# Kernel tuning notes

Hardware: AMD Instinct MI355X
Metric: run time of the kernel (lower is better)

The kernel has to match this reference:

```python
import jax, jax.numpy as jnp
import numpy as np

N, E, IN_C, HID, OUT_C, HEADS, NUM_CLASSES = 50000, 800000, 128, 64, 64, 4, 40
NEG_SLOPE = 0.2


def _gat_conv(x, src, dst, W, a_src, a_dst, bias, heads, concat):
    # x: [N, F_in]; W: [F_in, heads*C]; a_src/a_dst: [1, heads, C]; bias: [out]
    n = x.shape[0]
    h = (x @ W).reshape(n, heads, -1)                      # [N, H, C]
    alpha_s = (h * a_src).sum(-1)                          # [N, H]
    alpha_d = (h * a_dst).sum(-1)                          # [N, H]
    e = jax.nn.leaky_relu(alpha_s[src] + alpha_d[dst], NEG_SLOPE)  # [E, H]
    # scatter-softmax over incoming edges of each dst node
    emax = jax.ops.segment_max(e, dst, num_segments=n)
    emax = jnp.where(jnp.isfinite(emax), emax, 0.0)
    ee = jnp.exp(e - emax[dst])
    denom = jax.ops.segment_sum(ee, dst, num_segments=n) + 1e-16
    w = ee / denom[dst]                                    # [E, H]
    out = jax.ops.segment_sum(h[src] * w[:, :, None], dst, num_segments=n)  # [N, H, C]
    out = out.reshape(n, -1) if concat else out.mean(axis=1)
    return out + bias


def setup_inputs() -> dict:
    key = jax.random.key(0)
    ks = jax.random.split(key, 12)
    s1 = 1.0 / np.sqrt(IN_C)
    s2 = 1.0 / np.sqrt(HID * HEADS)
    s3 = 1.0 / np.sqrt(OUT_C)
    return {
        "x": jax.random.normal(ks[0], (N, IN_C), dtype=jnp.float32),
        "edge_index": jax.random.randint(ks[1], (2, E), 0, N, dtype=jnp.int64),
        "W1": jax.random.normal(ks[2], (IN_C, HEADS * HID), dtype=jnp.float32) * s1,
        "att_src1": jax.random.normal(ks[3], (1, HEADS, HID), dtype=jnp.float32) * s1,
        "att_dst1": jax.random.normal(ks[4], (1, HEADS, HID), dtype=jnp.float32) * s1,
        "b1": jnp.zeros((HEADS * HID,), dtype=jnp.float32),
        "W2": jax.random.normal(ks[5], (HEADS * HID, OUT_C), dtype=jnp.float32) * s2,
        "att_src2": jax.random.normal(ks[6], (1, 1, OUT_C), dtype=jnp.float32) * s2,
        "att_dst2": jax.random.normal(ks[7], (1, 1, OUT_C), dtype=jnp.float32) * s2,
        "b2": jnp.zeros((OUT_C,), dtype=jnp.float32),
        "fc_w": jax.random.normal(ks[8], (OUT_C, NUM_CLASSES), dtype=jnp.float32) * s3,
        "fc_b": jnp.zeros((NUM_CLASSES,), dtype=jnp.float32),
    }


def reference(x, edge_index, W1, att_src1, att_dst1, b1, W2, att_src2, att_dst2, b2, fc_w, fc_b):
    n = x.shape[0]
    loops = jnp.arange(n, dtype=edge_index.dtype)
    ei = jnp.concatenate([edge_index, jnp.stack([loops, loops])], axis=1)  # add self-loops (PyG default)
    src, dst = ei[0], ei[1]
    h = jax.nn.relu(_gat_conv(x, src, dst, W1, att_src1, att_dst1, b1, HEADS, True))
    h = jax.nn.relu(_gat_conv(h, src, dst, W2, att_src2, att_dst2, b2, 1, False))
    # dropout p=0.01 is identity in eval mode
    pooled = h.mean(axis=0, keepdims=True)                 # global mean pool -> [1, OUT_C]
    logits = pooled @ fc_w + fc_b
    return jax.nn.log_softmax(logits, axis=1)
```

## Files before the change

kernel.cpp:

```cpp
#include <hip/hip_runtime.h>
#include <hip/hip_bf16.h>
#include <math.h>

#define NEG_SLOPE 0.2f
#define CHUNK2 2048
#define PGROUPS 32

typedef __attribute__((ext_vector_type(8))) short bf16x8;
typedef __attribute__((ext_vector_type(4))) float f32x4;
typedef __attribute__((ext_vector_type(2))) float f32x2_t;

__device__ __forceinline__ float lrelu(float a) { return a >= 0.f ? a : NEG_SLOPE * a; }
__device__ __forceinline__ unsigned short f2bu(float v) {
  unsigned u = __float_as_uint(v);
  u += 0x7fffu + ((u >> 16) & 1u);
  return (unsigned short)(u >> 16);
}
__device__ __forceinline__ unsigned char f2fp8(float v) {
  return (unsigned char)(__builtin_amdgcn_cvt_pk_fp8_f32(v, v, 0, false) & 0xFF);
}
__device__ __forceinline__ void fp8x4_dec(unsigned v, float& a, float& b, float& c, float& d) {
  f32x2_t lo = __builtin_amdgcn_cvt_pk_f32_fp8(v, false);
  f32x2_t hi = __builtin_amdgcn_cvt_pk_f32_fp8(v, true);
  a = lo.x; b = lo.y; c = hi.x; d = hi.y;
}

__global__ __launch_bounds__(256) void prep_kernel(
    const float4* __restrict__ x4, ushort4* __restrict__ xb4, int nx4,
    const float* __restrict__ W1, unsigned short* __restrict__ w1t,
    const float* __restrict__ W2, unsigned short* __restrict__ w2t,
    const int* __restrict__ ei, int* __restrict__ bhist, int E0, int Etot, int NBUCK,
    int castBlocks, int wBlocks, int histBlocks) {
  __shared__ int hsm[256];
  int t = threadIdx.x;
  if (blockIdx.x < (unsigned)castBlocks) {
    for (int i = blockIdx.x * 256 + t; i < nx4; i += castBlocks * 256) {
      float4 v = x4[i];
      xb4[i] = make_ushort4(f2bu(v.x), f2bu(v.y), f2bu(v.z), f2bu(v.w));
    }
  } else if (blockIdx.x < (unsigned)(castBlocks + wBlocks)) {
    int bid = blockIdx.x - castBlocks;
    const int tot1 = 128 * 256, tot2 = 256 * 64;
    for (int i = bid * 256 + t; i < tot1 + tot2; i += wBlocks * 256) {
      if (i < tot1) { int k = i >> 8, n = i & 255; w1t[n * 128 + k] = f2bu(W1[i]); }
      else { int j = i - tot1; int k = j >> 6, n = j & 63; w2t[n * 256 + k] = f2bu(W2[j]); }
    }
  } else {
    int bid = blockIdx.x - castBlocks - wBlocks;
    hsm[t] = 0;
    __syncthreads();
    for (int e = bid * 256 + t; e < Etot; e += histBlocks * 256) {
      int dst = (e < E0) ? ei[E0 + e] : (e - E0);
      atomicAdd(&hsm[dst >> 8], 1);
    }
    __syncthreads();
    if (t < NBUCK && hsm[t]) atomicAdd(&bhist[t], hsm[t]);
  }
}

__global__ __launch_bounds__(256) void bucket_scan_kernel(const int* __restrict__ bhist,
    int* __restrict__ bucketOff, int* __restrict__ cursor, int* __restrict__ rowptrN,
    int NBUCK, int Etot) {
  __shared__ int s[256];
  int t = threadIdx.x;
  int v = (t < NBUCK) ? bhist[t] : 0;
  s[t] = v;
  __syncthreads();
  for (int off = 1; off < 256; off <<= 1) {
    int u = (t >= off) ? s[t - off] : 0;
    __syncthreads();
    s[t] += u;
    __syncthreads();
  }
  int excl = s[t] - v;
  if (t < NBUCK) { bucketOff[t] = excl; cursor[t] = excl; }
  if (t == 0) { bucketOff[NBUCK] = Etot; *rowptrN = Etot; }
}

__device__ void gemm_tile(const unsigned short* __restrict__ A,
    const unsigned short* __restrict__ BT, unsigned char* __restrict__ C8,
    const float* __restrict__ att_s, const float* __restrict__ att_d,
    float* __restrict__ as_, float* __restrict__ ad_,
    int M, int K, int Ncol, int H, int bx, int by, char* smem) {
  unsigned short (*Al)[40] = (unsigned short (*)[40])smem;
  unsigned short (*Bt)[40] = (unsigned short (*)[40])(smem + 5120);
  float* sal = (float*)(smem + 10240);
  float* sad = (float*)(smem + 10752);
  const int tid = threadIdx.x;
  const int row0 = by * 64, col0 = bx * 64;
  const int lane = tid & 63, wave = tid >> 6;
  const int wm = wave >> 1, wn = wave & 1;
  const int l15 = lane & 15, q = lane >> 4;

  f32x4 acc[2][2] = {};

  const int rr = tid >> 2, rc = (tid & 3) * 8;

  for (int k0 = 0; k0 < K; k0 += 32) {
    ushort4 av0 = make_ushort4(0, 0, 0, 0), av1 = av0;
    if (row0 + rr < M) {
      const ushort4* ap = (const ushort4*)(A + (size_t)(row0 + rr) * K + k0 + rc);
      av0 = ap[0]; av1 = ap[1];
    }
    *(ushort4*)&Al[rr][rc] = av0;
    *(ushort4*)&Al[rr][rc + 4] = av1;
    {
      const ushort4* bp = (const ushort4*)(BT + (size_t)(col0 + rr) * K + k0 + rc);
      *(ushort4*)&Bt[rr][rc] = bp[0];
      *(ushort4*)&Bt[rr][rc + 4] = bp[1];
    }
    __syncthreads();
    bf16x8 af[2], bf[2];
#pragma unroll
    for (int mi = 0; mi < 2; mi++)
      af[mi] = *(const bf16x8*)&Al[wm * 32 + mi * 16 + l15][q * 8];
#pragma unroll
    for (int ni = 0; ni < 2; ni++)
      bf[ni] = *(const bf16x8*)&Bt[wn * 32 + ni * 16 + l15][q * 8];
#pragma unroll
    for (int mi = 0; mi < 2; mi++)
#pragma unroll
      for (int ni = 0; ni < 2; ni++)
        acc[mi][ni] = __builtin_amdgcn_mfma_f32_16x16x32_bf16(af[mi], bf[ni], acc[mi][ni], 0, 0, 0);
    __syncthreads();
  }
#pragma unroll
  for (int mi = 0; mi < 2; mi++) {
#pragma unroll
    for (int r = 0; r < 4; r++) {
      int grow = row0 + wm * 32 + mi * 16 + q * 4 + r;
      if (grow < M) {
#pragma unroll
        for (int ni = 0; ni < 2; ni++) {
          int gcol = col0 + wn * 32 + ni * 16 + l15;
          C8[(size_t)grow * Ncol + gcol] = f2fp8(acc[mi][ni][r]);
        }
      }
    }
  }
  float atts0 = att_s[col0 + wn * 32 + l15];
  float atts1 = att_s[col0 + wn * 32 + 16 + l15];
  float attd0 = att_d[col0 + wn * 32 + l15];
  float attd1 = att_d[col0 + wn * 32 + 16 + l15];
#pragma unroll
  for (int mi = 0; mi < 2; mi++) {
#pragma unroll
    for (int r = 0; r < 4; r++) {
      float vs = acc[mi][0][r] * atts0 + acc[mi][1][r] * atts1;
      float vd = acc[mi][0][r] * attd0 + acc[mi][1][r] * attd1;
#pragma unroll
      for (int off = 1; off < 16; off <<= 1) {
        vs += __shfl_xor(vs, off);
        vd += __shfl_xor(vd, off);
      }
      if (l15 == 0) {
        int rl = wm * 32 + mi * 16 + q * 4 + r;
        sal[wn * 64 + rl] = vs;
        sad[wn * 64 + rl] = vd;
      }
    }
  }
  __syncthreads();
  if (tid < 64) {
    int grow = row0 + tid;
    if (grow < M) {
      as_[(size_t)grow * H + bx] = sal[tid] + sal[64 + tid];
      ad_[(size_t)grow * H + bx] = sad[tid] + sad[64 + tid];
    }
  }
}

__global__ __launch_bounds__(256) void gemm_alpha_kernel(const unsigned short* __restrict__ A,
    const unsigned short* __restrict__ BT, unsigned char* __restrict__ C8,
    const float* __restrict__ att_s, const float* __restrict__ att_d,
    float* __restrict__ as_, float* __restrict__ ad_, int M, int K, int Ncol, int H) {
  __shared__ __align__(16) char smem[11264];
  gemm_tile(A, BT, C8, att_s, att_d, as_, ad_, M, K, Ncol, H, blockIdx.x, blockIdx.y, smem);
}

__global__ __launch_bounds__(256) void gemm1_scatter_kernel(
    const unsigned short* __restrict__ A, const unsigned short* __restrict__ BT,
    unsigned char* __restrict__ C8, const float* __restrict__ att_s,
    const float* __restrict__ att_d, float* __restrict__ as_, float* __restrict__ ad_,
    int M, int K, int Ncol, int H, int GX,
    const int* __restrict__ ei, int* __restrict__ cursor, int* __restrict__ pairs,
    int E0, int Etot, int NBUCK, int NSC) {
  __shared__ __align__(16) char smem[18432];
  if (blockIdx.x < (unsigned)NSC) {
    int2* stage = (int2*)smem;
    int* h = (int*)(smem + 16384);
    int* base = (int*)(smem + 17408);
    int t = threadIdx.x;
    int e0 = blockIdx.x * CHUNK2;
    h[t] = 0;
    __syncthreads();
    int cnt = Etot - e0;
    if (cnt > CHUNK2) cnt = CHUNK2;
    for (int i = t; i < cnt; i += 256) {
      int e = e0 + i;
      int s, d;
      if (e < E0) { s = ei[e]; d = ei[E0 + e]; } else { s = d = e - E0; }
      stage[i] = make_int2((s << 8) | (d & 255), d >> 8);
      atomicAdd(&h[d >> 8], 1);
    }
    __syncthreads();
    if (t < NBUCK && h[t]) base[t] = atomicAdd(&cursor[t], h[t]);
    __syncthreads();
    for (int i = t; i < cnt; i += 256) {
      int2 p = stage[i];
      int pos = atomicAdd(&base[p.y], 1);
      pairs[pos] = p.x;
    }
  } else {
    int flat = blockIdx.x - NSC;
    gemm_tile(A, BT, C8, att_s, att_d, as_, ad_, M, K, Ncol, H, flat % GX, flat / GX, smem);
  }
}

__global__ __launch_bounds__(256) void csr_build_kernel(const int* __restrict__ pairs,
    const int* __restrict__ bucketOff, int* __restrict__ rowptr, int* __restrict__ csr_src,
    int N) {
  int b = blockIdx.x, t = threadIdx.x;
  int base = bucketOff[b], cnt = bucketOff[b + 1] - base;
  int n0 = b << 8;
  __shared__ int h[256];
  __shared__ int s[256];
  __shared__ int ex[256];
  h[t] = 0;
  __syncthreads();
  for (int i = t; i < cnt; i += 256) atomicAdd(&h[pairs[base + i] & 255], 1);
  __syncthreads();
  int v = h[t];
  s[t] = v;
  __syncthreads();
  for (int off = 1; off < 256; off <<= 1) {
    int u = (t >= off) ? s[t - off] : 0;
    __syncthreads();
    s[t] += u;
    __syncthreads();
  }
  ex[t] = s[t] - v;
  if (n0 + t < N) rowptr[n0 + t] = base + ex[t];
  __syncthreads();
  for (int i = t; i < cnt; i += 256) {
    int p = pairs[base + i];
    int pos = atomicAdd(&ex[p & 255], 1);
    csr_src[base + pos] = ((unsigned)p) >> 8;
  }
}

__global__ __launch_bounds__(256) void aggr1_kernel(const int* __restrict__ rowptr,
    const int* __restrict__ csr_src, const float* __restrict__ as_,
    const float* __restrict__ ad_, const uint4* __restrict__ h1f8,
    const float* __restrict__ b1, unsigned short* __restrict__ out1, int Nn) {
  int lane = threadIdx.x & 63, wv = threadIdx.x >> 6;
  int q = lane >> 4, l15 = lane & 15;
  int n = (blockIdx.x * 4 + wv) * 4 + q;
  if (n >= Nn) return;
  int row = rowptr[n], deg = rowptr[n + 1] - row;
  int hh = l15 >> 2;
  float adv = ad_[n * 4 + hh];
  const uint4* hb = h1f8 + l15;
  float acc[16] = {};
  float wsum = 0.f;
  int s = 0;
  for (; s + 2 <= deg; s += 2) {
    int i0 = csr_src[row + s], i1 = csr_src[row + s + 1];
    float a0v = as_[i0 * 4 + hh], a1v = as_[i1 * 4 + hh];
    uint4 x0 = hb[(size_t)i0 * 16];
    uint4 x1 = hb[(size_t)i1 * 16];
    float w0 = __expf(lrelu(a0v + adv));
    float w1 = __expf(lrelu(a1v + adv));
    wsum += w0 + w1;
    float c0, c1, c2, c3;
    fp8x4_dec(x0.x, c0, c1, c2, c3);
    acc[0] = fmaf(w0, c0, acc[0]); acc[1] = fmaf(w0, c1, acc[1]);
    acc[2] = fmaf(w0, c2, acc[2]); acc[3] = fmaf(w0, c3, acc[3]);
    fp8x4_dec(x0.y, c0, c1, c2, c3);
    acc[4] = fmaf(w0, c0, acc[4]); acc[5] = fmaf(w0, c1, acc[5]);
    acc[6] = fmaf(w0, c2, acc[6]); acc[7] = fmaf(w0, c3, acc[7]);
    fp8x4_dec(x0.z, c0, c1, c2, c3);
    acc[8] = fmaf(w0, c0, acc[8]); acc[9] = fmaf(w0, c1, acc[9]);
    acc[10] = fmaf(w0, c2, acc[10]); acc[11] = fmaf(w0, c3, acc[11]);
    fp8x4_dec(x0.w, c0, c1, c2, c3);
    acc[12] = fmaf(w0, c0, acc[12]); acc[13] = fmaf(w0, c1, acc[13]);
    acc[14] = fmaf(w0, c2, acc[14]); acc[15] = fmaf(w0, c3, acc[15]);
    fp8x4_dec(x1.x, c0, c1, c2, c3);
    acc[0] = fmaf(w1, c0, acc[0]); acc[1] = fmaf(w1, c1, acc[1]);
    acc[2] = fmaf(w1, c2, acc[2]); acc[3] = fmaf(w1, c3, acc[3]);
    fp8x4_dec(x1.y, c0, c1, c2, c3);
    acc[4] = fmaf(w1, c0, acc[4]); acc[5] = fmaf(w1, c1, acc[5]);
    acc[6] = fmaf(w1, c2, acc[6]); acc[7] = fmaf(w1, c3, acc[7]);
    fp8x4_dec(x1.z, c0, c1, c2, c3);
    acc[8] = fmaf(w1, c0, acc[8]); acc[9] = fmaf(w1, c1, acc[9]);
    acc[10] = fmaf(w1, c2, acc[10]); acc[11] = fmaf(w1, c3, acc[11]);
    fp8x4_dec(x1.w, c0, c1, c2, c3);
    acc[12] = fmaf(w1, c0, acc[12]); acc[13] = fmaf(w1, c1, acc[13]);
    acc[14] = fmaf(w1, c2, acc[14]); acc[15] = fmaf(w1, c3, acc[15]);
  }
  if (s < deg) {
    int i0 = csr_src[row + s];
    float w0 = __expf(lrelu(as_[i0 * 4 + hh] + adv));
    wsum += w0;
    uint4 x0 = hb[(size_t)i0 * 16];
    float c0, c1, c2, c3;
    fp8x4_dec(x0.x, c0, c1, c2, c3);
    acc[0] = fmaf(w0, c0, acc[0]); acc[1] = fmaf(w0, c1, acc[1]);
    acc[2] = fmaf(w0, c2, acc[2]); acc[3] = fmaf(w0, c3, acc[3]);
    fp8x4_dec(x0.y, c0, c1, c2, c3);
    acc[4] = fmaf(w0, c0, acc[4]); acc[5] = fmaf(w0, c1, acc[5]);
    acc[6] = fmaf(w0, c2, acc[6]); acc[7] = fmaf(w0, c3, acc[7]);
    fp8x4_dec(x0.z, c0, c1, c2, c3);
    acc[8] = fmaf(w0, c0, acc[8]); acc[9] = fmaf(w0, c1, acc[9]);
    acc[10] = fmaf(w0, c2, acc[10]); acc[11] = fmaf(w0, c3, acc[11]);
    fp8x4_dec(x0.w, c0, c1, c2, c3);
    acc[12] = fmaf(w0, c0, acc[12]); acc[13] = fmaf(w0, c1, acc[13]);
    acc[14] = fmaf(w0, c2, acc[14]); acc[15] = fmaf(w0, c3, acc[15]);
  }
  float vinv = 1.f / wsum;
  int c0i = l15 * 16;
  unsigned short ob[16];
#pragma unroll
  for (int k = 0; k < 4; k++) {
    float4 bb = *(const float4*)(b1 + c0i + k * 4);
    float r0 = fmaf(acc[k * 4 + 0], vinv, bb.x);
    float r1 = fmaf(acc[k * 4 + 1], vinv, bb.y);
    float r2 = fmaf(acc[k * 4 + 2], vinv, bb.z);
    float r3 = fmaf(acc[k * 4 + 3], vinv, bb.w);
    ob[k * 4 + 0] = f2bu(r0 > 0.f ? r0 : 0.f);
    ob[k * 4 + 1] = f2bu(r1 > 0.f ? r1 : 0.f);
    ob[k * 4 + 2] = f2bu(r2 > 0.f ? r2 : 0.f);
    ob[k * 4 + 3] = f2bu(r3 > 0.f ? r3 : 0.f);
  }
  *(ushort4*)(out1 + (size_t)n * 256 + c0i) = *(ushort4*)&ob[0];
  *(ushort4*)(out1 + (size_t)n * 256 + c0i + 4) = *(ushort4*)&ob[4];
  *(ushort4*)(out1 + (size_t)n * 256 + c0i + 8) = *(ushort4*)&ob[8];
  *(ushort4*)(out1 + (size_t)n * 256 + c0i + 12) = *(ushort4*)&ob[12];
}

__global__ __launch_bounds__(256) void aggr2_pool_kernel(const int* __restrict__ rowptr,
    const int* __restrict__ csr_src, const float* __restrict__ as_,
    const float* __restrict__ ad_, const unsigned* __restrict__ h2f8,
    const float* __restrict__ b2, float* __restrict__ pooled_grp, int Nn) {
  int lane = threadIdx.x & 63, wv = threadIdx.x >> 6;
  int q = lane >> 4, l15 = lane & 15;
  int c0 = l15 * 4;
  const unsigned* hb = h2f8 + l15;
  float p0 = 0.f, p1 = 0.f, p2 = 0.f, p3 = 0.f;
  int stream = (blockIdx.x * 4 + wv) * 4 + q;
  int nstreams = gridDim.x * 16;
  for (int n = stream; n < Nn; n += nstreams) {
    int row = rowptr[n], deg = rowptr[n + 1] - row;
    float adv = ad_[n];
    float a0 = 0.f, a1 = 0.f, a2 = 0.f, a3 = 0.f, wsum = 0.f;
    int s = 0;
    for (; s + 8 <= deg; s += 8) {
      int idx[8];
      float al[8];
      unsigned xv[8];
#pragma unroll
      for (int j = 0; j < 8; j++) idx[j] = csr_src[row + s + j];
#pragma unroll
      for (int j = 0; j < 8; j++) al[j] = as_[idx[j]];
#pragma unroll
      for (int j = 0; j < 8; j++) xv[j] = hb[(size_t)idx[j] * 16];
#pragma unroll
      for (int j = 0; j < 8; j++) {
        float w = __expf(lrelu(al[j] + adv));
        wsum += w;
        float c0f, c1f, c2f, c3f;
        fp8x4_dec(xv[j], c0f, c1f, c2f, c3f);
        a0 = fmaf(w, c0f, a0); a1 = fmaf(w, c1f, a1);
        a2 = fmaf(w, c2f, a2); a3 = fmaf(w, c3f, a3);
      }
    }
    if (s + 4 <= deg) {
      int idx[4];
      float al[4];
      unsigned xv[4];
#pragma unroll
      for (int j = 0; j < 4; j++) idx[j] = csr_src[row + s + j];
#pragma unroll
      for (int j = 0; j < 4; j++) al[j] = as_[idx[j]];
#pragma unroll
      for (int j = 0; j < 4; j++) xv[j] = hb[(size_t)idx[j] * 16];
#pragma unroll
      for (int j = 0; j < 4; j++) {
        float w = __expf(lrelu(al[j] + adv));
        wsum += w;
        float c0f, c1f, c2f, c3f;
        fp8x4_dec(xv[j], c0f, c1f, c2f, c3f);
        a0 = fmaf(w, c0f, a0); a1 = fmaf(w, c1f, a1);
        a2 = fmaf(w, c2f, a2); a3 = fmaf(w, c3f, a3);
      }
      s += 4;
    }
    for (; s < deg; s++) {
      int i0 = csr_src[row + s];
      float w = __expf(lrelu(as_[i0] + adv));
      wsum += w;
      float c0f, c1f, c2f, c3f;
      fp8x4_dec(hb[(size_t)i0 * 16], c0f, c1f, c2f, c3f);
      a0 = fmaf(w, c0f, a0); a1 = fmaf(w, c1f, a1);
      a2 = fmaf(w, c2f, a2); a3 = fmaf(w, c3f, a3);
    }
    float vinv = 1.f / wsum;
    float4 bb = *(const float4*)(b2 + c0);
    float r0 = fmaf(a0, vinv, bb.x), r1 = fmaf(a1, vinv, bb.y);
    float r2 = fmaf(a2, vinv, bb.z), r3 = fmaf(a3, vinv, bb.w);
    p0 += r0 > 0.f ? r0 : 0.f; p1 += r1 > 0.f ? r1 : 0.f;
    p2 += r2 > 0.f ? r2 : 0.f; p3 += r3 > 0.f ? r3 : 0.f;
  }
  __shared__ float4 sred[4][4][16];
  sred[wv][q][l15] = make_float4(p0, p1, p2, p3);
  __syncthreads();
  if (threadIdx.x < 64) {
    int slot = threadIdx.x >> 2, comp = threadIdx.x & 3;
    float acc = 0.f;
#pragma unroll
    for (int i = 0; i < 4; i++)
#pragma unroll
      for (int j = 0; j < 4; j++) {
        float4 v = sred[i][j][slot];
        acc += comp == 0 ? v.x : (comp == 1 ? v.y : (comp == 2 ? v.z : v.w));
      }
    atomicAdd(&pooled_grp[(blockIdx.x & (PGROUPS - 1)) * 64 + slot * 4 + comp], acc);
  }
}

__global__ __launch_bounds__(64) void pool_head_kernel(const float* __restrict__ pooled_grp,
    const float* __restrict__ fc_w, const float* __restrict__ fc_b,
    float* __restrict__ out, float invN) {
  int t = threadIdx.x;
  __shared__ float pl[64];
  __shared__ float lg[40];
  __shared__ float lse;
  float acc = 0.f;
#pragma unroll
  for (int g = 0; g < PGROUPS; g++) acc += pooled_grp[g * 64 + t];
  pl[t] = acc * invN;
  __syncthreads();
  if (t < 40) {
    float sm = fc_b[t];
    for (int c = 0; c < 64; c++) sm = fmaf(pl[c], fc_w[c * 40 + t], sm);
    lg[t] = sm;
  }
  __syncthreads();
  if (t == 0) {
    float m = -1e30f;
    for (int j = 0; j < 40; j++) m = fmaxf(m, lg[j]);
    float su = 0.f;
    for (int j = 0; j < 40; j++) su += expf(lg[j] - m);
    lse = m + logf(su);
  }
  __syncthreads();
  if (t < 40) out[t] = lg[t] - lse;
}

extern "C" void kernel_launch(void* const* d_in, const int* in_sizes, int n_in,
                              void* d_out, int out_size, void* d_ws, size_t ws_size,
                              hipStream_t stream) {
  const float* x        = (const float*)d_in[0];
  const int*   ei       = (const int*)d_in[1];
  const float* W1       = (const float*)d_in[2];
  const float* att_src1 = (const float*)d_in[3];
  const float* att_dst1 = (const float*)d_in[4];
  const float* b1       = (const float*)d_in[5];
  const float* W2       = (const float*)d_in[6];
  const float* att_src2 = (const float*)d_in[7];
  const float* att_dst2 = (const float*)d_in[8];
  const float* b2       = (const float*)d_in[9];
  const float* fc_w     = (const float*)d_in[10];
  const float* fc_b     = (const float*)d_in[11];
  float* out = (float*)d_out;

  const int N    = in_sizes[0] / 128;
  const int E0   = in_sizes[1] / 2;
  const int Etot = E0 + N;
  const int NBUCK = (N + 255) >> 8;
  const int NSC  = (Etot + CHUNK2 - 1) / CHUNK2;
  const int GBY  = (N + 63) / 64;
  const int AGG2_BLOCKS = 2048;

  char* wsb = (char*)d_ws;
  size_t o = 0;
  auto alloc = [&](size_t bytes) { char* p = wsb + o; o += (bytes + 15) & ~(size_t)15; return p; };
  unsigned short* xb   = (unsigned short*)alloc((size_t)N * 128 * 2);
  unsigned short* w1t  = (unsigned short*)alloc(256 * 128 * 2);
  unsigned short* w2t  = (unsigned short*)alloc(64 * 256 * 2);
  unsigned char*  h1f8 = (unsigned char*)alloc((size_t)N * 256);
  unsigned short* out1 = (unsigned short*)alloc((size_t)N * 256 * 2);
  float* as1  = (float*)alloc((size_t)N * 4 * 4);
  float* ad1  = (float*)alloc((size_t)N * 4 * 4);
  float* as2  = (float*)alloc((size_t)N * 4);
  float* ad2  = (float*)alloc((size_t)N * 4);
  int* rowptr = (int*)alloc((size_t)(N + 1) * 4);
  int* bhist  = (int*)alloc(256 * 4);
  int* bucketOff = (int*)alloc(257 * 4);
  int* cursor = (int*)alloc(256 * 4);
  int* pairs  = (int*)alloc((size_t)Etot * 4);
  int* csr_src = (int*)alloc((size_t)Etot * 4);
  float* pooled_grp = (float*)alloc((size_t)PGROUPS * 64 * 4);

  dim3 blk(256);

  hipMemsetAsync(bhist, 0, 256 * sizeof(int), stream);
  hipMemsetAsync(pooled_grp, 0, (size_t)PGROUPS * 64 * sizeof(float), stream);
  prep_kernel<<<512 + 16 + 256, blk, 0, stream>>>(
      (const float4*)x, (ushort4*)xb, N * 128 / 4,
      W1, w1t, W2, w2t,
      ei, bhist, E0, Etot, NBUCK, 512, 16, 256);
  bucket_scan_kernel<<<1, blk, 0, stream>>>(bhist, bucketOff, cursor, rowptr + N, NBUCK, Etot);

  gemm1_scatter_kernel<<<NSC + 4 * GBY, blk, 0, stream>>>(
      xb, w1t, h1f8, att_src1, att_dst1, as1, ad1, N, 128, 256, 4, 4,
      ei, cursor, pairs, E0, Etot, NBUCK, NSC);
  csr_build_kernel<<<NBUCK, blk, 0, stream>>>(pairs, bucketOff, rowptr, csr_src, N);

  aggr1_kernel<<<(N + 15) / 16, blk, 0, stream>>>(rowptr, csr_src, as1, ad1,
                                                  (const uint4*)h1f8, b1, out1, N);

  gemm_alpha_kernel<<<dim3(1, GBY), blk, 0, stream>>>(out1, w2t, h1f8, att_src2, att_dst2,
                                                      as2, ad2, N, 256, 64, 1);
  aggr2_pool_kernel<<<AGG2_BLOCKS, blk, 0, stream>>>(rowptr, csr_src, as2, ad2,
                                                     (const unsigned*)h1f8, b2, pooled_grp, N);

  pool_head_kernel<<<1, 64, 0, stream>>>(pooled_grp, fc_w, fc_b, out, 1.0f / (float)N);
}
```

Measured before the change: 223.6 us.

## Cooperatively load CSR indices via shuffles and unroll aggregation by four

```diff
diff --git a/kernel.cpp b/kernel.cpp
--- a/kernel.cpp
+++ b/kernel.cpp
@@ -60,7 +60,7 @@
 
 __global__ __launch_bounds__(256) void bucket_scan_kernel(const int* __restrict__ bhist,
     int* __restrict__ bucketOff, int* __restrict__ cursor, int* __restrict__ rowptrN,
-    int NBUCK, int Etot) {
+    float* __restrict__ pooled_grp, int NBUCK, int Etot) {
   __shared__ int s[256];
   int t = threadIdx.x;
   int v = (t < NBUCK) ? bhist[t] : 0;
@@ -75,6 +75,7 @@
   int excl = s[t] - v;
   if (t < NBUCK) { bucketOff[t] = excl; cursor[t] = excl; }
   if (t == 0) { bucketOff[NBUCK] = Etot; *rowptrN = Etot; }
+  for (int i = t; i < PGROUPS * 64; i += 256) pooled_grp[i] = 0.f;
 }
 
 __device__ void gemm_tile(const unsigned short* __restrict__ A,
@@ -249,6 +250,22 @@
   }
 }
 
+#define ACC16(W, X) do {                                                       \
+    float c0_, c1_, c2_, c3_;                                                  \
+    fp8x4_dec((X).x, c0_, c1_, c2_, c3_);                                      \
+    acc[0] = fmaf((W), c0_, acc[0]);  acc[1] = fmaf((W), c1_, acc[1]);         \
+    acc[2] = fmaf((W), c2_, acc[2]);  acc[3] = fmaf((W), c3_, acc[3]);         \
+    fp8x4_dec((X).y, c0_, c1_, c2_, c3_);                                      \
+    acc[4] = fmaf((W), c0_, acc[4]);  acc[5] = fmaf((W), c1_, acc[5]);         \
+    acc[6] = fmaf((W), c2_, acc[6]);  acc[7] = fmaf((W), c3_, acc[7]);         \
+    fp8x4_dec((X).z, c0_, c1_, c2_, c3_);                                      \
+    acc[8] = fmaf((W), c0_, acc[8]);  acc[9] = fmaf((W), c1_, acc[9]);         \
+    acc[10] = fmaf((W), c2_, acc[10]); acc[11] = fmaf((W), c3_, acc[11]);      \
+    fp8x4_dec((X).w, c0_, c1_, c2_, c3_);                                      \
+    acc[12] = fmaf((W), c0_, acc[12]); acc[13] = fmaf((W), c1_, acc[13]);      \
+    acc[14] = fmaf((W), c2_, acc[14]); acc[15] = fmaf((W), c3_, acc[15]);      \
+  } while (0)
+
 __global__ __launch_bounds__(256) void aggr1_kernel(const int* __restrict__ rowptr,
     const int* __restrict__ csr_src, const float* __restrict__ as_,
     const float* __restrict__ ad_, const uint4* __restrict__ h1f8,
@@ -258,64 +275,52 @@
   int n = (blockIdx.x * 4 + wv) * 4 + q;
   if (n >= Nn) return;
   int row = rowptr[n], deg = rowptr[n + 1] - row;
+  int rowEnd = row + deg;
   int hh = l15 >> 2;
   float adv = ad_[n * 4 + hh];
   const uint4* hb = h1f8 + l15;
   float acc[16] = {};
   float wsum = 0.f;
-  int s = 0;
-  for (; s + 2 <= deg; s += 2) {
-    int i0 = csr_src[row + s], i1 = csr_src[row + s + 1];
-    float a0v = as_[i0 * 4 + hh], a1v = as_[i1 * 4 + hh];
-    uint4 x0 = hb[(size_t)i0 * 16];
-    uint4 x1 = hb[(size_t)i1 * 16];
-    float w0 = __expf(lrelu(a0v + adv));
-    float w1 = __expf(lrelu(a1v + adv));
-    wsum += w0 + w1;
-    float c0, c1, c2, c3;
-    fp8x4_dec(x0.x, c0, c1, c2, c3);
-    acc[0] = fmaf(w0, c0, acc[0]); acc[1] = fmaf(w0, c1, acc[1]);
-    acc[2] = fmaf(w0, c2, acc[2]); acc[3] = fmaf(w0, c3, acc[3]);
-    fp8x4_dec(x0.y, c0, c1, c2, c3);
-    acc[4] = fmaf(w0, c0, acc[4]); acc[5] = fmaf(w0, c1, acc[5]);
-    acc[6] = fmaf(w0, c2, acc[6]); acc[7] = fmaf(w0, c3, acc[7]);
-    fp8x4_dec(x0.z, c0, c1, c2, c3);
-    acc[8] = fmaf(w0, c0, acc[8]); acc[9] = fmaf(w0, c1, acc[9]);
-    acc[10] = fmaf(w0, c2, acc[10]); acc[11] = fmaf(w0, c3, acc[11]);
-    fp8x4_dec(x0.w, c0, c1, c2, c3);
-    acc[12] = fmaf(w0, c0, acc[12]); acc[13] = fmaf(w0, c1, acc[13]);
-    acc[14] = fmaf(w0, c2, acc[14]); acc[15] = fmaf(w0, c3, acc[15]);
-    fp8x4_dec(x1.x, c0, c1, c2, c3);
-    acc[0] = fmaf(w1, c0, acc[0]); acc[1] = fmaf(w1, c1, acc[1]);
-    acc[2] = fmaf(w1, c2, acc[2]); acc[3] = fmaf(w1, c3, acc[3]);
-    fp8x4_dec(x1.y, c0, c1, c2, c3);
-    acc[4] = fmaf(w1, c0, acc[4]); acc[5] = fmaf(w1, c1, acc[5]);
-    acc[6] = fmaf(w1, c2, acc[6]); acc[7] = fmaf(w1, c3, acc[7]);
-    fp8x4_dec(x1.z, c0, c1, c2, c3);
-    acc[8] = fmaf(w1, c0, acc[8]); acc[9] = fmaf(w1, c1, acc[9]);
-    acc[10] = fmaf(w1, c2, acc[10]); acc[11] = fmaf(w1, c3, acc[11]);
-    fp8x4_dec(x1.w, c0, c1, c2, c3);
-    acc[12] = fmaf(w1, c0, acc[12]); acc[13] = fmaf(w1, c1, acc[13]);
-    acc[14] = fmaf(w1, c2, acc[14]); acc[15] = fmaf(w1, c3, acc[15]);
-  }
-  if (s < deg) {
-    int i0 = csr_src[row + s];
-    float w0 = __expf(lrelu(as_[i0 * 4 + hh] + adv));
-    wsum += w0;
-    uint4 x0 = hb[(size_t)i0 * 16];
-    float c0, c1, c2, c3;
-    fp8x4_dec(x0.x, c0, c1, c2, c3);
-    acc[0] = fmaf(w0, c0, acc[0]); acc[1] = fmaf(w0, c1, acc[1]);
-    acc[2] = fmaf(w0, c2, acc[2]); acc[3] = fmaf(w0, c3, acc[3]);
-    fp8x4_dec(x0.y, c0, c1, c2, c3);
-    acc[4] = fmaf(w0, c0, acc[4]); acc[5] = fmaf(w0, c1, acc[5]);
-    acc[6] = fmaf(w0, c2, acc[6]); acc[7] = fmaf(w0, c3, acc[7]);
-    fp8x4_dec(x0.z, c0, c1, c2, c3);
-    acc[8] = fmaf(w0, c0, acc[8]); acc[9] = fmaf(w0, c1, acc[9]);
-    acc[10] = fmaf(w0, c2, acc[10]); acc[11] = fmaf(w0, c3, acc[11]);
-    fp8x4_dec(x0.w, c0, c1, c2, c3);
-    acc[12] = fmaf(w0, c0, acc[12]); acc[13] = fmaf(w0, c1, acc[13]);
-    acc[14] = fmaf(w0, c2, acc[14]); acc[15] = fmaf(w0, c3, acc[15]);
+  int p0 = row + l15;
+  int idxv = (p0 < rowEnd) ? csr_src[p0] : 0;
+  for (int s0 = 0; s0 < deg; s0 += 16) {
+    int pn = row + s0 + 16 + l15;
+    int idxn = (pn < rowEnd) ? csr_src[pn] : 0;
+    int m = deg - s0;
+    if (m > 16) m = 16;
+    int j = 0;
+    for (; j + 4 <= m; j += 4) {
+      int i0 = __shfl(idxv, j, 16);
+      int i1 = __shfl(idxv, j + 1, 16);
+      int i2 = __shfl(idxv, j + 2, 16);
+      int i3 = __shfl(idxv, j + 3, 16);
+      float a0v = as_[i0 * 4 + hh];
+      float a1v = as_[i1 * 4 + hh];
+      float a2v = as_[i2 * 4 + hh];
+      float a3v = as_[i3 * 4 + hh];
+      uint4 x0 = hb[(size_t)i0 * 16];
+      uint4 x1 = hb[(size_t)i1 * 16];
+      uint4 x2 = hb[(size_t)i2 * 16];
+      uint4 x3 = hb[(size_t)i3 * 16];
+      float w0 = __expf(lrelu(a0v + adv));
+      float w1 = __expf(lrelu(a1v + adv));
+      float w2 = __expf(lrelu(a2v + adv));
+      float w3 = __expf(lrelu(a3v + adv));
+      wsum += (w0 + w1) + (w2 + w3);
+      ACC16(w0, x0);
+      ACC16(w1, x1);
+      ACC16(w2, x2);
+      ACC16(w3, x3);
+    }
+    for (; j < m; j++) {
+      int i0 = __shfl(idxv, j, 16);
+      float a0v = as_[i0 * 4 + hh];
+      uint4 x0 = hb[(size_t)i0 * 16];
+      float w0 = __expf(lrelu(a0v + adv));
+      wsum += w0;
+      ACC16(w0, x0);
+    }
+    idxv = idxn;
   }
   float vinv = 1.f / wsum;
   int c0i = l15 * 16;
@@ -351,58 +356,67 @@
   int nstreams = gridDim.x * 16;
   for (int n = stream; n < Nn; n += nstreams) {
     int row = rowptr[n], deg = rowptr[n + 1] - row;
+    int rowEnd = row + deg;
     float adv = ad_[n];
     float a0 = 0.f, a1 = 0.f, a2 = 0.f, a3 = 0.f, wsum = 0.f;
-    int s = 0;
-    for (; s + 8 <= deg; s += 8) {
-      int idx[8];
-      float al[8];
-      unsigned xv[8];
-#pragma unroll
-      for (int j = 0; j < 8; j++) idx[j] = csr_src[row + s + j];
-#pragma unroll
-      for (int j = 0; j < 8; j++) al[j] = as_[idx[j]];
-#pragma unroll
-      for (int j = 0; j < 8; j++) xv[j] = hb[(size_t)idx[j] * 16];
-#pragma unroll
-      for (int j = 0; j < 8; j++) {
-        float w = __expf(lrelu(al[j] + adv));
+    int pp = row + l15;
+    int idxv = (pp < rowEnd) ? csr_src[pp] : 0;
+    for (int s0 = 0; s0 < deg; s0 += 16) {
+      int pn = row + s0 + 16 + l15;
+      int idxn = (pn < rowEnd) ? csr_src[pn] : 0;
+      int m = deg - s0;
+      if (m > 16) m = 16;
+      int j = 0;
+      for (; j + 8 <= m; j += 8) {
+        int id[8];
+        float al[8];
+        unsigned xv[8];
+#pragma unroll
+        for (int u = 0; u < 8; u++) id[u] = __shfl(idxv, j + u, 16);
+#pragma unroll
+        for (int u = 0; u < 8; u++) al[u] = as_[id[u]];
+#pragma unroll
+        for (int u = 0; u < 8; u++) xv[u] = hb[(size_t)id[u] * 16];
+#pragma unroll
+        for (int u = 0; u < 8; u++) {
+          float w = __expf(lrelu(al[u] + adv));
+          wsum += w;
+          float c0f, c1f, c2f, c3f;
+          fp8x4_dec(xv[u], c0f, c1f, c2f, c3f);
+          a0 = fmaf(w, c0f, a0); a1 = fmaf(w, c1f, a1);
+          a2 = fmaf(w, c2f, a2); a3 = fmaf(w, c3f, a3);
+        }
+      }
+      for (; j + 4 <= m; j += 4) {
+        int id[4];
+        float al[4];
+        unsigned xv[4];
+#pragma unroll
+        for (int u = 0; u < 4; u++) id[u] = __shfl(idxv, j + u, 16);
+#pragma unroll
+        for (int u = 0; u < 4; u++) al[u] = as_[id[u]];
+#pragma unroll
+        for (int u = 0; u < 4; u++) xv[u] = hb[(size_t)id[u] * 16];
+#pragma unroll
+        for (int u = 0; u < 4; u++) {
+          float w = __expf(lrelu(al[u] + adv));
+          wsum += w;
+          float c0f, c1f, c2f, c3f;
+          fp8x4_dec(xv[u], c0f, c1f, c2f, c3f);
+          a0 = fmaf(w, c0f, a0); a1 = fmaf(w, c1f, a1);
+          a2 = fmaf(w, c2f, a2); a3 = fmaf(w, c3f, a3);
+        }
+      }
+      for (; j < m; j++) {
+        int i0 = __shfl(idxv, j, 16);
+        float w = __expf(lrelu(as_[i0] + adv));
         wsum += w;
         float c0f, c1f, c2f, c3f;
-        fp8x4_dec(xv[j], c0f, c1f, c2f, c3f);
+        fp8x4_dec(hb[(size_t)i0 * 16], c0f, c1f, c2f, c3f);
         a0 = fmaf(w, c0f, a0); a1 = fmaf(w, c1f, a1);
         a2 = fmaf(w, c2f, a2); a3 = fmaf(w, c3f, a3);
       }
-    }
-    if (s + 4 <= deg) {
-      int idx[4];
-      float al[4];
-      unsigned xv[4];
-#pragma unroll
-      for (int j = 0; j < 4; j++) idx[j] = csr_src[row + s + j];
-#pragma unroll
-      for (int j = 0; j < 4; j++) al[j] = as_[idx[j]];
-#pragma unroll
-      for (int j = 0; j < 4; j++) xv[j] = hb[(size_t)idx[j] * 16];
-#pragma unroll
-      for (int j = 0; j < 4; j++) {
-        float w = __expf(lrelu(al[j] + adv));
-        wsum += w;
-        float c0f, c1f, c2f, c3f;
-        fp8x4_dec(xv[j], c0f, c1f, c2f, c3f);
-        a0 = fmaf(w, c0f, a0); a1 = fmaf(w, c1f, a1);
-        a2 = fmaf(w, c2f, a2); a3 = fmaf(w, c3f, a3);
-      }
-      s += 4;
-    }
-    for (; s < deg; s++) {
-      int i0 = csr_src[row + s];
-      float w = __expf(lrelu(as_[i0] + adv));
-      wsum += w;
-      float c0f, c1f, c2f, c3f;
-      fp8x4_dec(hb[(size_t)i0 * 16], c0f, c1f, c2f, c3f);
-      a0 = fmaf(w, c0f, a0); a1 = fmaf(w, c1f, a1);
-      a2 = fmaf(w, c2f, a2); a3 = fmaf(w, c3f, a3);
+      idxv = idxn;
     }
     float vinv = 1.f / wsum;
     float4 bb = *(const float4*)(b2 + c0);
@@ -505,12 +519,12 @@
   dim3 blk(256);
 
   hipMemsetAsync(bhist, 0, 256 * sizeof(int), stream);
-  hipMemsetAsync(pooled_grp, 0, (size_t)PGROUPS * 64 * sizeof(float), stream);
   prep_kernel<<<512 + 16 + 256, blk, 0, stream>>>(
       (const float4*)x, (ushort4*)xb, N * 128 / 4,
       W1, w1t, W2, w2t,
       ei, bhist, E0, Etot, NBUCK, 512, 16, 256);
-  bucket_scan_kernel<<<1, blk, 0, stream>>>(bhist, bucketOff, cursor, rowptr + N, NBUCK, Etot);
+  bucket_scan_kernel<<<1, blk, 0, stream>>>(bhist, bucketOff, cursor, rowptr + N,
+                                            pooled_grp, NBUCK, Etot);
 
   gemm1_scatter_kernel<<<NSC + 4 * GBY, blk, 0, stream>>>(
       xb, w1t, h1f8, att_src1, att_dst1, as1, ad1, N, 128, 256, 4, 4,
```

Result: no change. 221.7 us (-0.9%).
